# Optimization experiments

Hardware: AMD Instinct MI355X
Metric: run time of the kernel (lower is better)

The kernel has to match this reference:

```python
import jax, jax.numpy as jnp
import numpy as np

B, N, D, H = 4, 2048, 256, 8
HD = D // H
E = 65536


def setup_inputs() -> dict:
    key = jax.random.key(0)
    ks = jax.random.split(key, 10)
    xav = lambda k, fi, fo: jax.random.uniform(k, (fo, fi), jnp.float32,
                                               -jnp.sqrt(6.0 / (fi + fo)), jnp.sqrt(6.0 / (fi + fo)))
    return {
        "x": jax.random.normal(ks[0], (B, N, D), jnp.float32),
        "edge_index": jax.random.randint(ks[1], (2, E), 0, N, jnp.int64 if jax.config.jax_enable_x64 else jnp.int32),
        "Wq": xav(ks[2], D, D), "bq": jnp.zeros((D,), jnp.float32),
        "Wk": xav(ks[3], D, D), "bk": jnp.zeros((D,), jnp.float32),
        "Wv": xav(ks[4], D, D), "bv": jnp.zeros((D,), jnp.float32),
        "Wo": xav(ks[5], D, D), "bo": jnp.zeros((D,), jnp.float32),
        "temperature": jnp.sqrt(jnp.float32(HD)),  # learned scalar, init sqrt(head_dim)
    }


def _build_mask(edge_index, num_nodes):
    # symmetric adjacency + self-loops; batch-independent -> build [N, N] once
    src, dst = edge_index[0], edge_index[1]
    adj = jnp.zeros((num_nodes, num_nodes), dtype=bool)
    adj = adj.at[src, dst].set(True).at[dst, src].set(True)
    diag = jnp.arange(num_nodes)
    return adj.at[diag, diag].set(True)


def reference(x, edge_index, Wq, bq, Wk, bk, Wv, bv, Wo, bo, temperature):
    b, n, d = x.shape
    def split(t):  # [B,N,D] -> [B,H,N,HD]
        return t.reshape(b, n, H, HD).transpose(0, 2, 1, 3)
    Q = split(x @ Wq.T + bq)
    K = split(x @ Wk.T + bk)
    V = split(x @ Wv.T + bv)
    scores = jnp.einsum('bhnd,bhmd->bhnm', Q, K) / temperature
    mask = _build_mask(edge_index, n)  # [N, N] bool, broadcasts over B, H
    scores = jnp.where(mask[None, None], scores, -jnp.inf)
    attn = jax.nn.softmax(scores, axis=-1)  # dropout = identity in eval
    attended = jnp.einsum('bhnm,bhmd->bhnd', attn, V)
    attended = attended.transpose(0, 2, 1, 3).reshape(b, n, d)
    out = attended @ Wo.T + bo  # output dropout = identity in eval
    return out, attn.mean(axis=1)
```

## Files before the change

kernel.cpp:

```cpp
#include <hip/hip_runtime.h>
#include <hip/hip_bf16.h>

#define BB 4
#define NN 2048
#define DD 256
#define HH 8
#define HDD 32
#define MASK_WORDS (NN / 32)
#define MAXDEG 192

typedef __hip_bfloat16 bf16;
typedef __attribute__((ext_vector_type(8))) short bf16x8;
typedef __attribute__((ext_vector_type(4))) float f32x4;

__device__ __forceinline__ float u16_to_bf16f(unsigned short w) {
    unsigned u = ((unsigned)w) << 16;
    return __uint_as_float(u);
}

__device__ __forceinline__ int detect_bf16(const unsigned short* tptr) {
    float t0 = u16_to_bf16f(tptr[0]);
    return (t0 > 1.0f && t0 < 16.0f) ? 1 : 0;
}

__device__ __forceinline__ float get_temp(const unsigned short* tptr, int isbf) {
    if (isbf) return u16_to_bf16f(tptr[0]);
    return ((const float*)tptr)[0];
}

__device__ __forceinline__ float ldf(const void* p, size_t i, int isbf) {
    if (isbf) return __bfloat162float(((const bf16*)p)[i]);
    return ((const float*)p)[i];
}

__device__ __forceinline__ void stf_nt(void* p, size_t i, float v, int isbf) {
    if (isbf) {
        bf16 h = __float2bfloat16(v);
        __builtin_nontemporal_store(*(unsigned short*)&h, (unsigned short*)p + i);
    } else {
        __builtin_nontemporal_store(v, (float*)p + i);
    }
}

__device__ __forceinline__ unsigned short bf16_hi(float x) {
    bf16 h = __float2bfloat16(x);
    return *(unsigned short*)&h;
}

__device__ __forceinline__ void split2(float a, float b, unsigned* hi, unsigned* lo) {
    unsigned short ha = bf16_hi(a), hb = bf16_hi(b);
    float ra = a - u16_to_bf16f(ha);
    float rb = b - u16_to_bf16f(hb);
    unsigned short la = bf16_hi(ra), lb = bf16_hi(rb);
    *hi = ((unsigned)hb << 16) | ha;
    *lo = ((unsigned)lb << 16) | la;
}

__global__ void build_mask_kernel(const unsigned* __restrict__ ei_raw, int E,
                                  unsigned* __restrict__ mask) {
    bool is64 = true;
    for (int i = 1; i < 16; i += 2) {
        if (ei_raw[i] != 0u) { is64 = false; break; }
    }
    int e = blockIdx.x * blockDim.x + threadIdx.x;
    if (e < E) {
        int s, d;
        if (is64) {
            s = (int)ei_raw[(size_t)2 * e];
            d = (int)ei_raw[(size_t)2 * (E + e)];
        } else {
            s = ((const int*)ei_raw)[e];
            d = ((const int*)ei_raw)[E + e];
        }
        atomicOr(&mask[(size_t)s * MASK_WORDS + (d >> 5)], 1u << (d & 31));
        atomicOr(&mask[(size_t)d * MASK_WORDS + (s >> 5)], 1u << (s & 31));
    }
    if (e < NN) {
        atomicOr(&mask[(size_t)e * MASK_WORDS + (e >> 5)], 1u << (e & 31));
    }
}

__global__ __launch_bounds__(64) void csr_kernel(const unsigned* __restrict__ mask,
                                                 unsigned short* __restrict__ nbr,
                                                 int* __restrict__ cnt) {
    int n = blockIdx.x;
    int t = threadIdx.x;
    unsigned w = mask[(size_t)n * MASK_WORDS + t];
    int pc = __popc(w);
    int pref = pc;
    for (int off = 1; off < 64; off <<= 1) {
        int o = __shfl_up(pref, off, 64);
        if (t >= off) pref += o;
    }
    int start = pref - pc;
    int total = __shfl(pref, 63, 64);
    unsigned ww = w;
    int pos = start;
    while (ww) {
        int bit = __ffs(ww) - 1;
        if (pos < MAXDEG) nbr[(size_t)n * MAXDEG + pos] = (unsigned short)(t * 32 + bit);
        pos++;
        ww &= ww - 1;
    }
    if (t == 0) cnt[n] = total > MAXDEG ? MAXDEG : total;
}

__global__ __launch_bounds__(256) void prep_weights(
        const void* __restrict__ W0, const void* __restrict__ W1,
        const void* __restrict__ W2, const void* __restrict__ W3,
        const unsigned short* __restrict__ tptr,
        unsigned* __restrict__ whi, unsigned* __restrict__ wlo) {
    int isbf = detect_bf16(tptr);
    int idx = blockIdx.x * 256 + threadIdx.x;
    int mat = idx >> 14;
    int off = (idx & 16383) * 4;
    const void* W = (mat == 0) ? W0 : (mat == 1) ? W1 : (mat == 2) ? W2 : W3;
    float f0 = ldf(W, off + 0, isbf), f1 = ldf(W, off + 1, isbf);
    float f2 = ldf(W, off + 2, isbf), f3 = ldf(W, off + 3, isbf);
    unsigned h0, l0, h1, l1;
    split2(f0, f1, &h0, &l0);
    split2(f2, f3, &h1, &l1);
    size_t w32 = ((size_t)mat * 65536 + off) >> 1;
    whi[w32] = h0; whi[w32 + 1] = h1;
    wlo[w32] = l0; wlo[w32 + 1] = l1;
}

__global__ __launch_bounds__(512) void proj_qkv_mfma(
        const void* __restrict__ X,
        const unsigned short* __restrict__ whi, const unsigned short* __restrict__ wlo,
        const void* __restrict__ bq, const void* __restrict__ bk, const void* __restrict__ bv,
        const unsigned short* __restrict__ tptr, float* __restrict__ QKV) {
    __shared__ __align__(16) char lds[32768];
    int isbf = detect_bf16(tptr);
    int tid = threadIdx.x;
    int row0 = blockIdx.x * 32;

    {
        int r = tid >> 4;
        int ec = (tid & 15) * 16;
        float f[16];
        if (!isbf) {
            const float* xp = (const float*)X + (size_t)(row0 + r) * DD + ec;
            float4 v0 = *(const float4*)xp;
            float4 v1 = *(const float4*)(xp + 4);
            float4 v2 = *(const float4*)(xp + 8);
            float4 v3 = *(const float4*)(xp + 12);
            f[0]=v0.x; f[1]=v0.y; f[2]=v0.z; f[3]=v0.w;
            f[4]=v1.x; f[5]=v1.y; f[6]=v1.z; f[7]=v1.w;
            f[8]=v2.x; f[9]=v2.y; f[10]=v2.z; f[11]=v2.w;
            f[12]=v3.x; f[13]=v3.y; f[14]=v3.z; f[15]=v3.w;
        } else {
#pragma unroll
            for (int e = 0; e < 16; e++) f[e] = ldf(X, (size_t)(row0 + r) * DD + ec + e, 1);
        }
        unsigned hp[8], lp[8];
#pragma unroll
        for (int e = 0; e < 8; e++) split2(f[2 * e], f[2 * e + 1], &hp[e], &lp[e]);
        int sw1 = ((ec * 2)      ^ ((r & 7) << 4));
        int sw2 = ((ec * 2 + 16) ^ ((r & 7) << 4));
        char* base = lds + r * 512;
        *(uint4*)(base + sw1) = make_uint4(hp[0], hp[1], hp[2], hp[3]);
        *(uint4*)(base + sw2) = make_uint4(hp[4], hp[5], hp[6], hp[7]);
        *(uint4*)(base + 16384 + sw1) = make_uint4(lp[0], lp[1], lp[2], lp[3]);
        *(uint4*)(base + 16384 + sw2) = make_uint4(lp[4], lp[5], lp[6], lp[7]);
    }
    __syncthreads();

    int lane = tid & 63, w = tid >> 6;
    int rA = lane & 15, kq = lane >> 4;
    int colbase = w * 32;

#pragma unroll
    for (int z = 0; z < 3; z++) {
        const unsigned short* Bh = whi + (size_t)z * 65536;
        const unsigned short* Bl = wlo + (size_t)z * 65536;
        const void* bias = (z == 0) ? bq : (z == 1) ? bk : bv;
        f32x4 acc00 = {0.f,0.f,0.f,0.f}, acc01 = {0.f,0.f,0.f,0.f};
        f32x4 acc10 = {0.f,0.f,0.f,0.f}, acc11 = {0.f,0.f,0.f,0.f};
#pragma unroll
        for (int ks = 0; ks < 8; ks++) {
            int sw = ((kq * 16 + ks * 64) ^ ((rA & 7) << 4));
            bf16x8 ah0 = *(const bf16x8*)(lds + rA * 512 + sw);
            bf16x8 ah1 = *(const bf16x8*)(lds + (16 + rA) * 512 + sw);
            bf16x8 al0 = *(const bf16x8*)(lds + 16384 + rA * 512 + sw);
            bf16x8 al1 = *(const bf16x8*)(lds + 16384 + (16 + rA) * 512 + sw);
            int koff = ks * 32 + kq * 8;
            bf16x8 bh0 = *(const bf16x8*)(Bh + (size_t)(colbase + rA) * DD + koff);
            bf16x8 bh1 = *(const bf16x8*)(Bh + (size_t)(colbase + 16 + rA) * DD + koff);
            bf16x8 bl0 = *(const bf16x8*)(Bl + (size_t)(colbase + rA) * DD + koff);
            bf16x8 bl1 = *(const bf16x8*)(Bl + (size_t)(colbase + 16 + rA) * DD + koff);
            acc00 = __builtin_amdgcn_mfma_f32_16x16x32_bf16(ah0, bh0, acc00, 0, 0, 0);
            acc00 = __builtin_amdgcn_mfma_f32_16x16x32_bf16(al0, bh0, acc00, 0, 0, 0);
            acc00 = __builtin_amdgcn_mfma_f32_16x16x32_bf16(ah0, bl0, acc00, 0, 0, 0);
            acc01 = __builtin_amdgcn_mfma_f32_16x16x32_bf16(ah0, bh1, acc01, 0, 0, 0);
            acc01 = __builtin_amdgcn_mfma_f32_16x16x32_bf16(al0, bh1, acc01, 0, 0, 0);
            acc01 = __builtin_amdgcn_mfma_f32_16x16x32_bf16(ah0, bl1, acc01, 0, 0, 0);
            acc10 = __builtin_amdgcn_mfma_f32_16x16x32_bf16(ah1, bh0, acc10, 0, 0, 0);
            acc10 = __builtin_amdgcn_mfma_f32_16x16x32_bf16(al1, bh0, acc10, 0, 0, 0);
            acc10 = __builtin_amdgcn_mfma_f32_16x16x32_bf16(ah1, bl0, acc10, 0, 0, 0);
            acc11 = __builtin_amdgcn_mfma_f32_16x16x32_bf16(ah1, bh1, acc11, 0, 0, 0);
            acc11 = __builtin_amdgcn_mfma_f32_16x16x32_bf16(al1, bh1, acc11, 0, 0, 0);
            acc11 = __builtin_amdgcn_mfma_f32_16x16x32_bf16(ah1, bl1, acc11, 0, 0, 0);
        }
        float* outz = QKV + (size_t)z * BB * NN * DD;
        float bv0 = ldf(bias, colbase + rA, isbf);
        float bv1 = ldf(bias, colbase + 16 + rA, isbf);
#pragma unroll
        for (int j = 0; j < 4; j++) {
            int r0 = row0 + kq * 4 + j;
            int r1 = r0 + 16;
            outz[(size_t)r0 * DD + colbase + rA]      = acc00[j] + bv0;
            outz[(size_t)r0 * DD + colbase + 16 + rA] = acc01[j] + bv1;
            outz[(size_t)r1 * DD + colbase + rA]      = acc10[j] + bv0;
            outz[(size_t)r1 * DD + colbase + 16 + rA] = acc11[j] + bv1;
        }
    }
}

__global__ __launch_bounds__(512) void out_proj_mfma(
        const unsigned short* __restrict__ Ahi, const unsigned short* __restrict__ Alo,
        const unsigned short* __restrict__ whi, const unsigned short* __restrict__ wlo,
        const void* __restrict__ bo, const unsigned short* __restrict__ tptr,
        void* __restrict__ out) {
    int isbf = detect_bf16(tptr);
    int tid = threadIdx.x;
    int row0 = blockIdx.x * 32;
    int lane = tid & 63, w = tid >> 6;
    int rA = lane & 15, kq = lane >> 4;
    int colbase = w * 32;
    const unsigned short* Bh = whi + (size_t)3 * 65536;
    const unsigned short* Bl = wlo + (size_t)3 * 65536;
    f32x4 acc00 = {0.f,0.f,0.f,0.f}, acc01 = {0.f,0.f,0.f,0.f};
    f32x4 acc10 = {0.f,0.f,0.f,0.f}, acc11 = {0.f,0.f,0.f,0.f};
#pragma unroll
    for (int ks = 0; ks < 8; ks++) {
        int koff = ks * 32 + kq * 8;
        bf16x8 ah0 = *(const bf16x8*)(Ahi + (size_t)(row0 + rA) * DD + koff);
        bf16x8 ah1 = *(const bf16x8*)(Ahi + (size_t)(row0 + 16 + rA) * DD + koff);
        bf16x8 al0 = *(const bf16x8*)(Alo + (size_t)(row0 + rA) * DD + koff);
        bf16x8 al1 = *(const bf16x8*)(Alo + (size_t)(row0 + 16 + rA) * DD + koff);
        bf16x8 bh0 = *(const bf16x8*)(Bh + (size_t)(colbase + rA) * DD + koff);
        bf16x8 bh1 = *(const bf16x8*)(Bh + (size_t)(colbase + 16 + rA) * DD + koff);
        bf16x8 bl0 = *(const bf16x8*)(Bl + (size_t)(colbase + rA) * DD + koff);
        bf16x8 bl1 = *(const bf16x8*)(Bl + (size_t)(colbase + 16 + rA) * DD + koff);
        acc00 = __builtin_amdgcn_mfma_f32_16x16x32_bf16(ah0, bh0, acc00, 0, 0, 0);
        acc00 = __builtin_amdgcn_mfma_f32_16x16x32_bf16(al0, bh0, acc00, 0, 0, 0);
        acc00 = __builtin_amdgcn_mfma_f32_16x16x32_bf16(ah0, bl0, acc00, 0, 0, 0);
        acc01 = __builtin_amdgcn_mfma_f32_16x16x32_bf16(ah0, bh1, acc01, 0, 0, 0);
        acc01 = __builtin_amdgcn_mfma_f32_16x16x32_bf16(al0, bh1, acc01, 0, 0, 0);
        acc01 = __builtin_amdgcn_mfma_f32_16x16x32_bf16(ah0, bl1, acc01, 0, 0, 0);
        acc10 = __builtin_amdgcn_mfma_f32_16x16x32_bf16(ah1, bh0, acc10, 0, 0, 0);
        acc10 = __builtin_amdgcn_mfma_f32_16x16x32_bf16(al1, bh0, acc10, 0, 0, 0);
        acc10 = __builtin_amdgcn_mfma_f32_16x16x32_bf16(ah1, bl0, acc10, 0, 0, 0);
        acc11 = __builtin_amdgcn_mfma_f32_16x16x32_bf16(ah1, bh1, acc11, 0, 0, 0);
        acc11 = __builtin_amdgcn_mfma_f32_16x16x32_bf16(al1, bh1, acc11, 0, 0, 0);
        acc11 = __builtin_amdgcn_mfma_f32_16x16x32_bf16(ah1, bl1, acc11, 0, 0, 0);
    }
    float bv0 = ldf(bo, colbase + rA, isbf);
    float bv1 = ldf(bo, colbase + 16 + rA, isbf);
#pragma unroll
    for (int j = 0; j < 4; j++) {
        int r0 = row0 + kq * 4 + j;
        int r1 = r0 + 16;
        stf_nt(out, (size_t)r0 * DD + colbase + rA,      acc00[j] + bv0, isbf);
        stf_nt(out, (size_t)r0 * DD + colbase + 16 + rA, acc01[j] + bv1, isbf);
        stf_nt(out, (size_t)r1 * DD + colbase + rA,      acc10[j] + bv0, isbf);
        stf_nt(out, (size_t)r1 * DD + colbase + 16 + rA, acc11[j] + bv1, isbf);
    }
}

__global__ __launch_bounds__(256, 8) void attn_kernel(
        const float* __restrict__ Q, const float* __restrict__ K,
        const float* __restrict__ V,
        const unsigned short* __restrict__ nbr_g, const int* __restrict__ cnt_g,
        const unsigned short* __restrict__ tptr,
        unsigned short* __restrict__ Ahi, unsigned short* __restrict__ Alo,
        void* __restrict__ out ) {
    __shared__ float sc[HH][MAXDEG + 1];
    __shared__ float part[4][DD];
    __shared__ float meanrow[NN];
    __shared__ unsigned short nbr_s[MAXDEG];
    __shared__ float invs[HH];

    int tid = threadIdx.x;
    int bid = blockIdx.x;
    int xcd = bid & 7;
    int b = xcd >> 1;
    int n = ((bid >> 3) << 1) | (xcd & 1);
    int g = tid >> 5;
    int lane32 = tid & 31;
    int r8 = lane32 >> 2;
    int dq = lane32 & 3;

    int isbf = detect_bf16(tptr);
    float inv_temp = 1.0f / get_temp(tptr, isbf);

    int C = cnt_g[n];
    if (C > MAXDEG) C = MAXDEG;

    for (int i = tid; i < NN; i += 256) meanrow[i] = 0.f;
    for (int i = tid; i < C; i += 256) nbr_s[i] = nbr_g[(size_t)n * MAXDEG + i];

    const float* qp = Q + (size_t)(b * NN + n) * DD + g * HDD + dq * 8;
    float4 q0 = *(const float4*)qp;
    float4 q1 = *(const float4*)(qp + 4);

    __syncthreads();

    const float* Kb = K + (size_t)b * NN * DD;
    const float* Vb = V + (size_t)b * NN * DD;

    for (int i0 = 0; i0 < C; i0 += 8) {
        int idx = i0 + r8;
        int m = nbr_s[idx < C ? idx : 0];
        const float* kp = Kb + (size_t)m * DD + g * HDD + dq * 8;
        float4 k0 = *(const float4*)kp;
        float4 k1 = *(const float4*)(kp + 4);
        float p = q0.x * k0.x + q0.y * k0.y + q0.z * k0.z + q0.w * k0.w
                + q1.x * k1.x + q1.y * k1.y + q1.z * k1.z + q1.w * k1.w;
        p += __shfl_xor(p, 1, 32);
        p += __shfl_xor(p, 2, 32);
        if (dq == 0 && idx < C) sc[g][idx] = p * inv_temp;
    }

    float lmax = -1e30f;
    for (int i = lane32; i < C; i += 32) lmax = fmaxf(lmax, sc[g][i]);
#pragma unroll
    for (int off = 16; off; off >>= 1) lmax = fmaxf(lmax, __shfl_xor(lmax, off, 32));
    float lsum = 0.f;
    for (int i = lane32; i < C; i += 32) {
        float pe = __expf(sc[g][i] - lmax);
        sc[g][i] = pe;
        lsum += pe;
    }
#pragma unroll
    for (int off = 16; off; off >>= 1) lsum += __shfl_xor(lsum, off, 32);
    float inv = 1.0f / fmaxf(lsum, 1e-30f);
    if (lane32 == 0) invs[g] = inv;

    __syncthreads();

    int w = tid >> 6;
    int l64 = tid & 63;
    int g2 = l64 >> 3;
    float4 vacc = {0.f, 0.f, 0.f, 0.f};
    for (int i = w; i < C; i += 4) {
        int m = nbr_s[i];
        float pp = sc[g2][i];
        float4 vv = *(const float4*)(Vb + (size_t)m * DD + l64 * 4);
        vacc.x = fmaf(pp, vv.x, vacc.x);
        vacc.y = fmaf(pp, vv.y, vacc.y);
        vacc.z = fmaf(pp, vv.z, vacc.z);
        vacc.w = fmaf(pp, vv.w, vacc.w);
    }
    *(float4*)&part[w][l64 * 4] = vacc;

    __syncthreads();

    {
        float s = part[0][tid] + part[1][tid] + part[2][tid] + part[3][tid];
        float a = s * invs[tid >> 5];
        size_t arow = (size_t)(b * NN + n) * DD + tid;
        unsigned short hu = bf16_hi(a);
        float resid = a - u16_to_bf16f(hu);
        unsigned short lu = bf16_hi(resid);
        __builtin_nontemporal_store(hu, Ahi + arow);
        __builtin_nontemporal_store(lu, Alo + arow);
    }

    for (int k = tid; k < C; k += 256) {
        float s8 = 0.f;
#pragma unroll
        for (int gg = 0; gg < HH; gg++) s8 += sc[gg][k] * invs[gg];
        meanrow[nbr_s[k]] = s8 * 0.125f;
    }
    __syncthreads();

    size_t obase = (size_t)BB * NN * DD + (size_t)(b * NN + n) * NN;
    for (int m = tid; m < NN; m += 256) stf_nt(out, obase + m, meanrow[m], isbf);
}

extern "C" void kernel_launch(void* const* d_in, const int* in_sizes, int n_in,
                              void* d_out, int out_size, void* d_ws, size_t ws_size,
                              hipStream_t stream) {
    const void* x  = d_in[0];
    const unsigned* ei = (const unsigned*)d_in[1];
    const void* Wq = d_in[2];
    const void* bq = d_in[3];
    const void* Wk = d_in[4];
    const void* bk = d_in[5];
    const void* Wv = d_in[6];
    const void* bv = d_in[7];
    const void* Wo = d_in[8];
    const void* bo = d_in[9];
    const unsigned short* tptr = (const unsigned short*)d_in[10];

    int E = in_sizes[1] / 2;

    char* ws = (char*)d_ws;
    unsigned* mask = (unsigned*)ws;
    float* Qw  = (float*)(ws + (size_t)NN * MASK_WORDS * 4);
    float* Kw  = Qw + (size_t)BB * NN * DD;
    float* Vw  = Kw + (size_t)BB * NN * DD;
    unsigned short* Ahi = (unsigned short*)(Vw + (size_t)BB * NN * DD);
    unsigned short* Alo = Ahi + (size_t)BB * NN * DD;
    unsigned* whi = (unsigned*)(Alo + (size_t)BB * NN * DD);
    unsigned* wlo = whi + (size_t)4 * 65536 / 2;
    unsigned short* nbr = (unsigned short*)(wlo + (size_t)4 * 65536 / 2);
    int* cnt = (int*)(nbr + (size_t)NN * MAXDEG);

    hipMemsetAsync(mask, 0, (size_t)NN * MASK_WORDS * 4, stream);

    int mth = (E > NN ? E : NN);
    build_mask_kernel<<<(mth + 255) / 256, 256, 0, stream>>>(ei, E, mask);
    csr_kernel<<<NN, 64, 0, stream>>>(mask, nbr, cnt);
    prep_weights<<<256, 256, 0, stream>>>(Wq, Wk, Wv, Wo, tptr, whi, wlo);

    proj_qkv_mfma<<<256, 512, 0, stream>>>(
        x, (const unsigned short*)whi, (const unsigned short*)wlo,
        bq, bk, bv, tptr, Qw);

    attn_kernel<<<BB * NN, 256, 0, stream>>>(Qw, Kw, Vw, nbr, cnt, tptr, Ahi, Alo, d_out);

    out_proj_mfma<<<256, 512, 0, stream>>>(
        Ahi, Alo, (const unsigned short*)whi, (const unsigned short*)wlo,
        bo, tptr, d_out);
}
```

Measured before the change: 211.1 us.

## Merge setup kernels, vectorize attn mean stores, and unroll PV accumulation

Folds mask building and weight splitting into one launch, and the CSR conversion and QKV projection into another, which removes two kernel launches and their serialization gaps. Inside the attention kernel, the mean-row zeroing and final writes now use 4-wide vector accesses, and the P·V loop is unrolled by two with separate accumulators so more loads are in flight. The risk is that the CSR blocks now share a launch with projection blocks that use 32KB of LDS and 512 threads, and the extra accumulator adds register pressure.

```diff
diff --git a/kernel.cpp b/kernel.cpp
--- a/kernel.cpp
+++ b/kernel.cpp
@@ -12,6 +12,7 @@
 typedef __hip_bfloat16 bf16;
 typedef __attribute__((ext_vector_type(8))) short bf16x8;
 typedef __attribute__((ext_vector_type(4))) float f32x4;
+typedef __attribute__((ext_vector_type(2))) unsigned u32x2;
 
 __device__ __forceinline__ float u16_to_bf16f(unsigned short w) {
     unsigned u = ((unsigned)w) << 16;
@@ -56,84 +57,90 @@
     *lo = ((unsigned)lb << 16) | la;
 }
 
-__global__ void build_mask_kernel(const unsigned* __restrict__ ei_raw, int E,
-                                  unsigned* __restrict__ mask) {
-    bool is64 = true;
-    for (int i = 1; i < 16; i += 2) {
-        if (ei_raw[i] != 0u) { is64 = false; break; }
-    }
-    int e = blockIdx.x * blockDim.x + threadIdx.x;
-    if (e < E) {
-        int s, d;
-        if (is64) {
-            s = (int)ei_raw[(size_t)2 * e];
-            d = (int)ei_raw[(size_t)2 * (E + e)];
-        } else {
-            s = ((const int*)ei_raw)[e];
-            d = ((const int*)ei_raw)[E + e];
-        }
-        atomicOr(&mask[(size_t)s * MASK_WORDS + (d >> 5)], 1u << (d & 31));
-        atomicOr(&mask[(size_t)d * MASK_WORDS + (s >> 5)], 1u << (s & 31));
-    }
-    if (e < NN) {
-        atomicOr(&mask[(size_t)e * MASK_WORDS + (e >> 5)], 1u << (e & 31));
-    }
-}
-
-__global__ __launch_bounds__(64) void csr_kernel(const unsigned* __restrict__ mask,
-                                                 unsigned short* __restrict__ nbr,
-                                                 int* __restrict__ cnt) {
-    int n = blockIdx.x;
-    int t = threadIdx.x;
-    unsigned w = mask[(size_t)n * MASK_WORDS + t];
-    int pc = __popc(w);
-    int pref = pc;
-    for (int off = 1; off < 64; off <<= 1) {
-        int o = __shfl_up(pref, off, 64);
-        if (t >= off) pref += o;
-    }
-    int start = pref - pc;
-    int total = __shfl(pref, 63, 64);
-    unsigned ww = w;
-    int pos = start;
-    while (ww) {
-        int bit = __ffs(ww) - 1;
-        if (pos < MAXDEG) nbr[(size_t)n * MAXDEG + pos] = (unsigned short)(t * 32 + bit);
-        pos++;
-        ww &= ww - 1;
-    }
-    if (t == 0) cnt[n] = total > MAXDEG ? MAXDEG : total;
-}
-
-__global__ __launch_bounds__(256) void prep_weights(
+__global__ __launch_bounds__(256) void mask_prep_kernel(
+        const unsigned* __restrict__ ei_raw, int E, int EB,
+        unsigned* __restrict__ mask,
         const void* __restrict__ W0, const void* __restrict__ W1,
         const void* __restrict__ W2, const void* __restrict__ W3,
         const unsigned short* __restrict__ tptr,
         unsigned* __restrict__ whi, unsigned* __restrict__ wlo) {
-    int isbf = detect_bf16(tptr);
-    int idx = blockIdx.x * 256 + threadIdx.x;
-    int mat = idx >> 14;
-    int off = (idx & 16383) * 4;
-    const void* W = (mat == 0) ? W0 : (mat == 1) ? W1 : (mat == 2) ? W2 : W3;
-    float f0 = ldf(W, off + 0, isbf), f1 = ldf(W, off + 1, isbf);
-    float f2 = ldf(W, off + 2, isbf), f3 = ldf(W, off + 3, isbf);
-    unsigned h0, l0, h1, l1;
-    split2(f0, f1, &h0, &l0);
-    split2(f2, f3, &h1, &l1);
-    size_t w32 = ((size_t)mat * 65536 + off) >> 1;
-    whi[w32] = h0; whi[w32 + 1] = h1;
-    wlo[w32] = l0; wlo[w32 + 1] = l1;
-}
-
-__global__ __launch_bounds__(512) void proj_qkv_mfma(
+    int bid = blockIdx.x;
+    int tid = threadIdx.x;
+    if (bid < EB) {
+        bool is64 = true;
+        for (int i = 1; i < 16; i += 2) {
+            if (ei_raw[i] != 0u) { is64 = false; break; }
+        }
+        int e = bid * 256 + tid;
+        if (e < E) {
+            int s, d;
+            if (is64) {
+                s = (int)ei_raw[(size_t)2 * e];
+                d = (int)ei_raw[(size_t)2 * (E + e)];
+            } else {
+                s = ((const int*)ei_raw)[e];
+                d = ((const int*)ei_raw)[E + e];
+            }
+            atomicOr(&mask[(size_t)s * MASK_WORDS + (d >> 5)], 1u << (d & 31));
+            atomicOr(&mask[(size_t)d * MASK_WORDS + (s >> 5)], 1u << (s & 31));
+        }
+        if (e < NN) {
+            atomicOr(&mask[(size_t)e * MASK_WORDS + (e >> 5)], 1u << (e & 31));
+        }
+    } else {
+        int isbf = detect_bf16(tptr);
+        int idx = (bid - EB) * 256 + tid;
+        int mat = idx >> 14;
+        int off = (idx & 16383) * 4;
+        const void* W = (mat == 0) ? W0 : (mat == 1) ? W1 : (mat == 2) ? W2 : W3;
+        float f0 = ldf(W, off + 0, isbf), f1 = ldf(W, off + 1, isbf);
+        float f2 = ldf(W, off + 2, isbf), f3 = ldf(W, off + 3, isbf);
+        unsigned h0, l0, h1, l1;
+        split2(f0, f1, &h0, &l0);
+        split2(f2, f3, &h1, &l1);
+        size_t w32 = ((size_t)mat * 65536 + off) >> 1;
+        whi[w32] = h0; whi[w32 + 1] = h1;
+        wlo[w32] = l0; wlo[w32 + 1] = l1;
+    }
+}
+
+__global__ __launch_bounds__(512) void csr_proj_kernel(
+        const unsigned* __restrict__ mask,
+        unsigned short* __restrict__ nbr, int* __restrict__ cnt,
         const void* __restrict__ X,
         const unsigned short* __restrict__ whi, const unsigned short* __restrict__ wlo,
         const void* __restrict__ bq, const void* __restrict__ bk, const void* __restrict__ bv,
         const unsigned short* __restrict__ tptr, float* __restrict__ QKV) {
     __shared__ __align__(16) char lds[32768];
+    int tid = threadIdx.x;
+    int bid = blockIdx.x;
+
+    if (bid >= 256) {
+        int n = ((bid - 256) << 3) | (tid >> 6);
+        int t = tid & 63;
+        unsigned w = mask[(size_t)n * MASK_WORDS + t];
+        int pc = __popc(w);
+        int pref = pc;
+        for (int off = 1; off < 64; off <<= 1) {
+            int o = __shfl_up(pref, off, 64);
+            if (t >= off) pref += o;
+        }
+        int start = pref - pc;
+        int total = __shfl(pref, 63, 64);
+        unsigned ww = w;
+        int pos = start;
+        while (ww) {
+            int bit = __ffs(ww) - 1;
+            if (pos < MAXDEG) nbr[(size_t)n * MAXDEG + pos] = (unsigned short)(t * 32 + bit);
+            pos++;
+            ww &= ww - 1;
+        }
+        if (t == 0) cnt[n] = total > MAXDEG ? MAXDEG : total;
+        return;
+    }
+
     int isbf = detect_bf16(tptr);
-    int tid = threadIdx.x;
-    int row0 = blockIdx.x * 32;
+    int row0 = bid * 32;
 
     {
         int r = tid >> 4;
@@ -278,7 +285,7 @@
         void* __restrict__ out ) {
     __shared__ float sc[HH][MAXDEG + 1];
     __shared__ float part[4][DD];
-    __shared__ float meanrow[NN];
+    __shared__ __align__(16) float meanrow[NN];
     __shared__ unsigned short nbr_s[MAXDEG];
     __shared__ float invs[HH];
 
@@ -298,7 +305,8 @@
     int C = cnt_g[n];
     if (C > MAXDEG) C = MAXDEG;
 
-    for (int i = tid; i < NN; i += 256) meanrow[i] = 0.f;
+    f32x4* mr4 = (f32x4*)meanrow;
+    for (int i = tid; i < NN / 4; i += 256) mr4[i] = (f32x4){0.f, 0.f, 0.f, 0.f};
     for (int i = tid; i < C; i += 256) nbr_s[i] = nbr_g[(size_t)n * MAXDEG + i];
 
     const float* qp = Q + (size_t)(b * NN + n) * DD + g * HDD + dq * 8;
@@ -343,17 +351,29 @@
     int w = tid >> 6;
     int l64 = tid & 63;
     int g2 = l64 >> 3;
-    float4 vacc = {0.f, 0.f, 0.f, 0.f};
-    for (int i = w; i < C; i += 4) {
-        int m = nbr_s[i];
-        float pp = sc[g2][i];
-        float4 vv = *(const float4*)(Vb + (size_t)m * DD + l64 * 4);
-        vacc.x = fmaf(pp, vv.x, vacc.x);
-        vacc.y = fmaf(pp, vv.y, vacc.y);
-        vacc.z = fmaf(pp, vv.z, vacc.z);
-        vacc.w = fmaf(pp, vv.w, vacc.w);
-    }
-    *(float4*)&part[w][l64 * 4] = vacc;
+    const float* scg = sc[g2];
+    float4 vacc0 = {0.f, 0.f, 0.f, 0.f};
+    float4 vacc1 = {0.f, 0.f, 0.f, 0.f};
+    int i = w;
+    for (; i + 4 < C; i += 8) {
+        int ma = nbr_s[i], mb2 = nbr_s[i + 4];
+        float pa = scg[i], pb = scg[i + 4];
+        float4 va = *(const float4*)(Vb + (size_t)ma * DD + l64 * 4);
+        float4 vb = *(const float4*)(Vb + (size_t)mb2 * DD + l64 * 4);
+        vacc0.x = fmaf(pa, va.x, vacc0.x); vacc0.y = fmaf(pa, va.y, vacc0.y);
+        vacc0.z = fmaf(pa, va.z, vacc0.z); vacc0.w = fmaf(pa, va.w, vacc0.w);
+        vacc1.x = fmaf(pb, vb.x, vacc1.x); vacc1.y = fmaf(pb, vb.y, vacc1.y);
+        vacc1.z = fmaf(pb, vb.z, vacc1.z); vacc1.w = fmaf(pb, vb.w, vacc1.w);
+    }
+    if (i < C) {
+        int ma = nbr_s[i];
+        float pa = scg[i];
+        float4 va = *(const float4*)(Vb + (size_t)ma * DD + l64 * 4);
+        vacc0.x = fmaf(pa, va.x, vacc0.x); vacc0.y = fmaf(pa, va.y, vacc0.y);
+        vacc0.z = fmaf(pa, va.z, vacc0.z); vacc0.w = fmaf(pa, va.w, vacc0.w);
+    }
+    vacc0.x += vacc1.x; vacc0.y += vacc1.y; vacc0.z += vacc1.z; vacc0.w += vacc1.w;
+    *(float4*)&part[w][l64 * 4] = vacc0;
 
     __syncthreads();
 
@@ -377,7 +397,21 @@
     __syncthreads();
 
     size_t obase = (size_t)BB * NN * DD + (size_t)(b * NN + n) * NN;
-    for (int m = tid; m < NN; m += 256) stf_nt(out, obase + m, meanrow[m], isbf);
+    if (isbf) {
+        unsigned short* ob = (unsigned short*)out + obase;
+        for (int m4 = tid; m4 < NN / 4; m4 += 256) {
+            f32x4 v = mr4[m4];
+            u32x2 uu;
+            uu[0] = ((unsigned)bf16_hi(v[1]) << 16) | bf16_hi(v[0]);
+            uu[1] = ((unsigned)bf16_hi(v[3]) << 16) | bf16_hi(v[2]);
+            __builtin_nontemporal_store(uu, (u32x2*)(ob + (size_t)m4 * 4));
+        }
+    } else {
+        float* ob = (float*)out + obase;
+        for (int m4 = tid; m4 < NN / 4; m4 += 256) {
+            __builtin_nontemporal_store(mr4[m4], (f32x4*)ob + m4);
+        }
+    }
 }
 
 extern "C" void kernel_launch(void* const* d_in, const int* in_sizes, int n_in,
@@ -412,12 +446,12 @@
     hipMemsetAsync(mask, 0, (size_t)NN * MASK_WORDS * 4, stream);
 
     int mth = (E > NN ? E : NN);
-    build_mask_kernel<<<(mth + 255) / 256, 256, 0, stream>>>(ei, E, mask);
-    csr_kernel<<<NN, 64, 0, stream>>>(mask, nbr, cnt);
-    prep_weights<<<256, 256, 0, stream>>>(Wq, Wk, Wv, Wo, tptr, whi, wlo);
-
-    proj_qkv_mfma<<<256, 512, 0, stream>>>(
-        x, (const unsigned short*)whi, (const unsigned short*)wlo,
+    int EB = (mth + 255) / 256;
+    mask_prep_kernel<<<EB + 256, 256, 0, stream>>>(ei, E, EB, mask,
+                                                   Wq, Wk, Wv, Wo, tptr, whi, wlo);
+
+    csr_proj_kernel<<<512, 512, 0, stream>>>(
+        mask, nbr, cnt, x, (const unsigned short*)whi, (const unsigned short*)wlo,
         bq, bk, bv, tptr, Qw);
 
     attn_kernel<<<BB * NN, 256, 0, stream>>>(Qw, Kw, Vw, nbr, cnt, tptr, Ahi, Alo, d_out);
```

After: 202.9 us. 3.9% less time.
